# Kernel tuning notes

Hardware: AMD Instinct MI355X
Metric: run time of the kernel (lower is better)

The kernel has to match this reference:

```python
import jax, jax.numpy as jnp
import numpy as np

D = 768
H = 12
MLP = 3072
EPS = 1e-5


def _layernorm(x, g, b):
    mu = jnp.mean(x, axis=-1, keepdims=True)
    var = jnp.var(x, axis=-1, keepdims=True)
    return (x - mu) * jax.lax.rsqrt(var + EPS) * g + b


def setup_inputs() -> dict:
    key = jax.random.key(0)
    ks = jax.random.split(key, 16)
    s = 0.02
    inp = {
        "x": jax.random.normal(ks[0], (8, 1024, D), dtype=jnp.float32),
        "ln1_g": jnp.ones((D,), jnp.float32),
        "ln1_b": jnp.zeros((D,), jnp.float32),
        "Wq": jax.random.normal(ks[1], (D, D), jnp.float32) * s,
        "bq": jnp.zeros((D,), jnp.float32),
        "Wk": jax.random.normal(ks[2], (D, D), jnp.float32) * s,
        "bk": jnp.zeros((D,), jnp.float32),
        "Wv": jax.random.normal(ks[3], (D, D), jnp.float32) * s,
        "bv": jnp.zeros((D,), jnp.float32),
        "Wo": jax.random.normal(ks[4], (D, D), jnp.float32) * s,
        "bo": jnp.zeros((D,), jnp.float32),
        "ln2_g": jnp.ones((D,), jnp.float32),
        "ln2_b": jnp.zeros((D,), jnp.float32),
        "W1": jax.random.normal(ks[5], (D, MLP), jnp.float32) * s,
        "b1": jnp.zeros((MLP,), jnp.float32),
        "W2": jax.random.normal(ks[6], (MLP, D), jnp.float32) * s,
        "b2": jnp.zeros((D,), jnp.float32),
    }
    return inp


def reference(x, ln1_g, ln1_b, Wq, bq, Wk, bk, Wv, bv, Wo, bo, ln2_g, ln2_b, W1, b1, W2, b2):
    b, n, d = x.shape
    dh = d // H
    scale = 1.0 / jnp.sqrt(jnp.float32(d))  # NOTE: sqrt(input_dim), per source

    h = _layernorm(x, ln1_g, ln1_b)
    q = (h @ Wq + bq).reshape(b, n, H, dh).transpose(0, 2, 1, 3)  # bhnf
    k = (h @ Wk + bk).reshape(b, n, H, dh).transpose(0, 2, 1, 3)
    v = (h @ Wv + bv).reshape(b, n, H, dh).transpose(0, 2, 1, 3)

    score = jax.nn.softmax(jnp.einsum('bhif,bhjf->bhij', q, k) * scale, axis=-1)
    attn = jnp.einsum('bhij,bhjf->bihf', score, v).reshape(b, n, d)
    out = attn @ Wo + bo + x  # residual (dropout p=0)

    h2 = _layernorm(out, ln2_g, ln2_b)
    mlp = jax.nn.gelu(jax.nn.gelu(h2 @ W1 + b1, approximate=False) @ W2 + b2, approximate=False)
    return mlp + out
```

## Files before the change

kernel.cpp:

```cpp
#include <hip/hip_runtime.h>
#include <hip/hip_bf16.h>
#include <math.h>

typedef __bf16 bf16x8 __attribute__((ext_vector_type(8)));
typedef float f32x4 __attribute__((ext_vector_type(4)));

#define DD 768
#define HH 12
#define MLPD 3072
#define QSCALE 0.036084391824351615f

__device__ __forceinline__ float gelu_fast(float x) {
    float y = 1.5957691216057308f * x + 0.07135481283154893f * x * x * x;
    return x * __builtin_amdgcn_rcpf(1.0f + __expf(-y));
}

__device__ __forceinline__ void gload16(const void* g, void* l) {
    __builtin_amdgcn_global_load_lds(
        (const __attribute__((address_space(1))) unsigned int*)g,
        (__attribute__((address_space(3))) unsigned int*)l, 16, 0, 0);
}

__global__ __launch_bounds__(256) void wtrans_all(
    const float* __restrict__ Wq, const float* __restrict__ Wk,
    const float* __restrict__ Wv, const float* __restrict__ Wo,
    const float* __restrict__ W1, const float* __restrict__ W2,
    __bf16* __restrict__ wqkv, __bf16* __restrict__ wo,
    __bf16* __restrict__ w1, __bf16* __restrict__ w2) {
    __shared__ float tile[64][65];
    int b = blockIdx.x;
    const float* W; __bf16* Wt; int K, N, tk, tn;
    if (b < 432) {
        int wsel = b / 144, r = b - wsel * 144;
        W = wsel == 0 ? Wq : (wsel == 1 ? Wk : Wv);
        Wt = wqkv + (size_t)wsel * 768 * 768;
        K = 768; N = 768; tk = r % 12; tn = r / 12;
    } else if (b < 576) {
        int r = b - 432; W = Wo; Wt = wo; K = 768; N = 768; tk = r % 12; tn = r / 12;
    } else if (b < 1152) {
        int r = b - 576; W = W1; Wt = w1; K = 768; N = 3072; tk = r % 12; tn = r / 12;
    } else {
        int r = b - 1152; W = W2; Wt = w2; K = 3072; N = 768; tk = r % 48; tn = r / 48;
    }
    int k0 = tk * 64, n0 = tn * 64;
    int t = threadIdx.x;
    int tr = t >> 6, tc = t & 63;
#pragma unroll
    for (int i = 0; i < 16; ++i) {
        int row = i * 4 + tr;
        tile[row][tc] = W[(size_t)(k0 + row) * N + n0 + tc];
    }
    __syncthreads();
#pragma unroll
    for (int i = 0; i < 16; ++i) {
        int row = i * 4 + tr;
        Wt[(size_t)(n0 + row) * K + k0 + tc] = (__bf16)tile[tc][row];
    }
}

__global__ __launch_bounds__(64) void ln_kernel(const float* __restrict__ X,
                                                const float* __restrict__ g,
                                                const float* __restrict__ b,
                                                __bf16* __restrict__ O) {
    int row = blockIdx.x;
    int lane = threadIdx.x;
    const float* xr = X + (size_t)row * DD;
    float4 v[3];
    float s = 0.f, ss = 0.f;
#pragma unroll
    for (int i = 0; i < 3; ++i) {
        v[i] = *reinterpret_cast<const float4*>(&xr[(i * 64 + lane) * 4]);
        s += v[i].x + v[i].y + v[i].z + v[i].w;
        ss += v[i].x * v[i].x + v[i].y * v[i].y + v[i].z * v[i].z + v[i].w * v[i].w;
    }
#pragma unroll
    for (int m = 1; m < 64; m <<= 1) {
        s += __shfl_xor(s, m);
        ss += __shfl_xor(ss, m);
    }
    float mu = s * (1.0f / DD);
    float rstd = rsqrtf(ss * (1.0f / DD) - mu * mu + 1e-5f);
#pragma unroll
    for (int i = 0; i < 3; ++i) {
        int c = (i * 64 + lane) * 4;
        float4 gv = *reinterpret_cast<const float4*>(&g[c]);
        float4 bv = *reinterpret_cast<const float4*>(&b[c]);
        union { __bf16 h[4]; uint2 u; } o;
        o.h[0] = (__bf16)((v[i].x - mu) * rstd * gv.x + bv.x);
        o.h[1] = (__bf16)((v[i].y - mu) * rstd * gv.y + bv.y);
        o.h[2] = (__bf16)((v[i].z - mu) * rstd * gv.z + bv.z);
        o.h[3] = (__bf16)((v[i].w - mu) * rstd * gv.w + bv.w);
        *reinterpret_cast<uint2*>(&O[(size_t)row * DD + c]) = o.u;
    }
}

template <int EPI>
__global__ __launch_bounds__(512, 2) void gemm8(
    const __bf16* __restrict__ A, const __bf16* __restrict__ Bt,
    const float* __restrict__ b0, const float* __restrict__ b1, const float* __restrict__ b2,
    void* __restrict__ o0, void* __restrict__ o1, void* __restrict__ o2,
    int M, int N, int K) {
    extern __shared__ __bf16 lds[];
    __bf16* As = lds;
    __bf16* Bs = lds + 49152;
    const int t = threadIdx.x;
    const int w = t >> 6, lane = t & 63;
    const int wm = w >> 1, wn = w & 1;
    const int lr = lane & 15, lg = lane >> 4;
    const int m0 = blockIdx.x * 256, n0 = blockIdx.y * 128;
    const int lrow8 = lane >> 3;
    const int cSwz = ((lane & 7) ^ lrow8) * 8;

    const __bf16* aSrc = A + (size_t)(m0 + w * 32 + lrow8) * K + cSwz;
    const __bf16* bSrc = Bt + (size_t)(n0 + w * 16 + lrow8) * K + cSwz;
    const int ldsA = w * 32 * 64;
    const int ldsB = w * 16 * 64;

    const int nt = K >> 6;
    f32x4 acc[4][4] = {};

    auto stageA = [&](int T, int c) {
        gload16(aSrc + (size_t)(c * 8) * K + T * 64,
                &As[(T % 3) * 16384 + ldsA + c * 8 * 64]);
    };
    auto stageB = [&](int T, int c) {
        gload16(bSrc + (size_t)(c * 8) * K + T * 64,
                &Bs[(T % 3) * 8192 + ldsB + c * 8 * 64]);
    };

    for (int T = 0; T < 2; ++T) {
        stageA(T, 0); stageA(T, 1); stageA(T, 2); stageA(T, 3);
        stageB(T, 0); stageB(T, 1);
    }
    asm volatile("s_waitcnt vmcnt(6)" ::: "memory");
    __builtin_amdgcn_s_barrier();

    for (int T = 0; T < nt; ++T) {
        const int bufA = (T % 3) * 16384, bufB = (T % 3) * 8192;
#pragma unroll
        for (int kg = 0; kg < 2; ++kg) {
            bf16x8 af[4], bfr[4];
#pragma unroll
            for (int i = 0; i < 4; ++i)
                af[i] = *reinterpret_cast<const bf16x8*>(
                    &As[bufA + (wm * 64 + i * 16 + lr) * 64 + (((kg << 2) | lg) ^ (lr & 7)) * 8]);
#pragma unroll
            for (int j = 0; j < 4; ++j)
                bfr[j] = *reinterpret_cast<const bf16x8*>(
                    &Bs[bufB + (wn * 64 + j * 16 + lr) * 64 + (((kg << 2) | lg) ^ (lr & 7)) * 8]);
            if (T + 2 < nt) {
                stageA(T + 2, kg * 2); stageA(T + 2, kg * 2 + 1); stageB(T + 2, kg);
            }
            __builtin_amdgcn_s_barrier();
            asm volatile("s_waitcnt lgkmcnt(0)" ::: "memory");
            __builtin_amdgcn_sched_barrier(0);
            __builtin_amdgcn_s_setprio(1);
#pragma unroll
            for (int i = 0; i < 4; ++i)
#pragma unroll
                for (int j = 0; j < 4; ++j)
                    acc[i][j] = __builtin_amdgcn_mfma_f32_16x16x32_bf16(bfr[j], af[i], acc[i][j], 0, 0, 0);
            __builtin_amdgcn_s_setprio(0);
            if (kg == 1) {
                if (T < nt - 2) { asm volatile("s_waitcnt vmcnt(6)" ::: "memory"); }
                else            { asm volatile("s_waitcnt vmcnt(0)" ::: "memory"); }
            }
            __builtin_amdgcn_s_barrier();
        }
    }

#pragma unroll
    for (int i = 0; i < 4; ++i) {
        const int m = m0 + wm * 64 + i * 16 + lr;
        const int bI = m >> 10, ntok = m & 1023;
#pragma unroll
        for (int j = 0; j < 4; ++j) {
            const int n = n0 + wn * 64 + j * 16 + lg * 4;
            if (EPI == 0) {
                const int wid = n / 768;
                const int cc0 = n - wid * 768;
                const int hh = cc0 >> 6, f0 = cc0 & 63;
                const float* bsel = (wid == 0 ? b0 : (wid == 1 ? b1 : b2));
                const float4 bv = *reinterpret_cast<const float4*>(&bsel[cc0]);
                const float v0 = acc[i][j][0] + bv.x, v1 = acc[i][j][1] + bv.y;
                const float v2 = acc[i][j][2] + bv.z, v3 = acc[i][j][3] + bv.w;
                if (wid == 0) {
                    union { __bf16 h[4]; uint2 u; } pk;
                    pk.h[0] = (__bf16)(v0 * QSCALE); pk.h[1] = (__bf16)(v1 * QSCALE);
                    pk.h[2] = (__bf16)(v2 * QSCALE); pk.h[3] = (__bf16)(v3 * QSCALE);
                    *reinterpret_cast<uint2*>(
                        &((__bf16*)o0)[((((size_t)(bI * HH + hh) << 10) + ntok) << 6) + f0]) = pk.u;
                } else if (wid == 1) {
                    union { __bf16 h[4]; uint2 u; } pk;
                    pk.h[0] = (__bf16)v0; pk.h[1] = (__bf16)v1;
                    pk.h[2] = (__bf16)v2; pk.h[3] = (__bf16)v3;
                    *reinterpret_cast<uint2*>(
                        &((__bf16*)o1)[((((size_t)(bI * HH + hh) << 10) + ntok) << 6) + f0]) = pk.u;
                } else {
                    __bf16* vb = (__bf16*)o2;
                    size_t base = ((size_t)(bI * HH + hh) * 64 + f0) << 10;
                    vb[base + ntok] = (__bf16)v0;
                    vb[base + (1 << 10) + ntok] = (__bf16)v1;
                    vb[base + (2 << 10) + ntok] = (__bf16)v2;
                    vb[base + (3 << 10) + ntok] = (__bf16)v3;
                }
            } else {
                const float4 bv = *reinterpret_cast<const float4*>(&b0[n]);
                union { __bf16 h[4]; uint2 u; } pk;
                pk.h[0] = (__bf16)gelu_fast(acc[i][j][0] + bv.x);
                pk.h[1] = (__bf16)gelu_fast(acc[i][j][1] + bv.y);
                pk.h[2] = (__bf16)gelu_fast(acc[i][j][2] + bv.z);
                pk.h[3] = (__bf16)gelu_fast(acc[i][j][3] + bv.w);
                *reinterpret_cast<uint2*>(&((__bf16*)o0)[(size_t)m * MLPD + n]) = pk.u;
            }
        }
    }
}

template <int EPI, int BM>
__global__ __launch_bounds__(256) void gemm_bt(
    const __bf16* __restrict__ A, const __bf16* __restrict__ Bt,
    const float* __restrict__ b0, void* __restrict__ o0,
    const float* __restrict__ resid, int M, int N, int K) {
    constexpr int WCOLS = (BM == 128) ? 2 : 4;
    constexpr int SPAN = 128 / WCOLS;
    constexpr int NJ = SPAN / 16;
    __shared__ __bf16 As[BM * 64];
    __shared__ __bf16 Bs[128 * 64];
    const int t = threadIdx.x;
    const int m0 = blockIdx.x * BM, n0 = blockIdx.y * 128;
    const int w = t >> 6, lane = t & 63;
    const int wm = w / WCOLS, wn = w % WCOLS;
    const int lr = lane & 15, lg = lane >> 4;

    const int srow = w * 8 + (lane >> 3);
    const int scol = (lane & 7) * 8;
    const __bf16* aP = A + (size_t)(m0 + srow) * K + scol;
    const __bf16* bP = Bt + (size_t)(n0 + srow) * K + scol;
    const int lbase = w * 8 * 64;

    f32x4 acc[4][NJ] = {};

    for (int k0 = 0; k0 < K; k0 += 64) {
        __syncthreads();
#pragma unroll
        for (int c = 0; c < BM / 32; ++c)
            gload16(aP + (size_t)c * 32 * K + k0, &As[lbase + c * 2048]);
#pragma unroll
        for (int c = 0; c < 4; ++c)
            gload16(bP + (size_t)c * 32 * K + k0, &Bs[lbase + c * 2048]);
        __syncthreads();
#pragma unroll
        for (int kg = 0; kg < 2; ++kg) {
            bf16x8 af[4], bfr[NJ];
#pragma unroll
            for (int i = 0; i < 4; ++i)
                af[i] = *reinterpret_cast<const bf16x8*>(&As[(wm * 64 + i * 16 + lr) * 64 + kg * 32 + lg * 8]);
#pragma unroll
            for (int j = 0; j < NJ; ++j)
                bfr[j] = *reinterpret_cast<const bf16x8*>(&Bs[(wn * SPAN + j * 16 + lr) * 64 + kg * 32 + lg * 8]);
#pragma unroll
            for (int i = 0; i < 4; ++i)
#pragma unroll
                for (int j = 0; j < NJ; ++j)
                    acc[i][j] = __builtin_amdgcn_mfma_f32_16x16x32_bf16(bfr[j], af[i], acc[i][j], 0, 0, 0);
        }
    }

#pragma unroll
    for (int i = 0; i < 4; ++i) {
        const int m = m0 + wm * 64 + i * 16 + lr;
#pragma unroll
        for (int j = 0; j < NJ; ++j) {
            const int n = n0 + wn * SPAN + j * 16 + lg * 4;
            const float4 bv = *reinterpret_cast<const float4*>(&b0[n]);
            const float v0 = acc[i][j][0] + bv.x, v1 = acc[i][j][1] + bv.y;
            const float v2 = acc[i][j][2] + bv.z, v3 = acc[i][j][3] + bv.w;
            const float4 rv = *reinterpret_cast<const float4*>(&resid[(size_t)m * DD + n]);
            if (EPI == 2) {
                float4 ov = {v0 + rv.x, v1 + rv.y, v2 + rv.z, v3 + rv.w};
                *reinterpret_cast<float4*>(&((float*)o0)[(size_t)m * DD + n]) = ov;
            } else {
                float4 ov = {gelu_fast(v0) + rv.x, gelu_fast(v1) + rv.y,
                             gelu_fast(v2) + rv.z, gelu_fast(v3) + rv.w};
                *reinterpret_cast<float4*>(&((float*)o0)[(size_t)m * DD + n]) = ov;
            }
        }
    }
}

__global__ __launch_bounds__(512, 6) void attn_kernel(
    const __bf16* __restrict__ Q, const __bf16* __restrict__ Kg,
    const __bf16* __restrict__ Vt, __bf16* __restrict__ Aout) {
    __shared__ char KsB[2][64 * 128];
    __shared__ char VsB[2][64 * 128];
    __shared__ char PsB[8][16 * 128];
    const int id = blockIdx.x;
    const int swz = (id & 7) * 96 + (id >> 3);
    const int bh = swz >> 3, qt = swz & 7;
    const int t = threadIdx.x, w = t >> 6, lane = t & 63;
    const int lr = lane & 15, lg = lane >> 4;
    const size_t bhN = (size_t)bh << 10;
    const int q0 = qt * 128;

    bf16x8 qf[2];
#pragma unroll
    for (int kg = 0; kg < 2; ++kg)
        qf[kg] = *reinterpret_cast<const bf16x8*>(&Q[(bhN + q0 + w * 16 + lr) * 64 + kg * 32 + lg * 8]);

    const int srow = t >> 3;
    const int sc = ((t & 7) ^ (srow & 7)) * 16;
    const char* kbase = (const char*)Kg + bhN * 128;
    const char* vbase = (const char*)Vt + ((size_t)bh << 17);
    const int wlds = w * 1024;

    f32x4 oacc[4] = {};
    float lsum[4] = {0.f, 0.f, 0.f, 0.f};

    gload16(kbase + (size_t)srow * 128 + sc, KsB[0] + wlds);
    gload16(vbase + (size_t)srow * 2048 + sc, VsB[0] + wlds);

    for (int kt = 0; kt < 16; ++kt) {
        const int buf = kt & 1;
        if (kt < 15) {
            gload16(kbase + (size_t)((kt + 1) * 64 + srow) * 128 + sc, KsB[buf ^ 1] + wlds);
            gload16(vbase + (size_t)srow * 2048 + (kt + 1) * 128 + sc, VsB[buf ^ 1] + wlds);
            asm volatile("s_waitcnt vmcnt(2)" ::: "memory");
        } else {
            asm volatile("s_waitcnt vmcnt(0)" ::: "memory");
        }
        __builtin_amdgcn_s_barrier();

        f32x4 s[4] = {};
        __builtin_amdgcn_s_setprio(1);
#pragma unroll
        for (int kg = 0; kg < 2; ++kg) {
#pragma unroll
            for (int j = 0; j < 4; ++j) {
                int row = j * 16 + lr;
                bf16x8 kf = *reinterpret_cast<const bf16x8*>(
                    KsB[buf] + ((row * 128 + kg * 64 + lg * 16) ^ ((row & 7) << 4)));
                s[j] = __builtin_amdgcn_mfma_f32_16x16x32_bf16(qf[kg], kf, s[j], 0, 0, 0);
            }
        }
        __builtin_amdgcn_s_setprio(0);
#pragma unroll
        for (int r = 0; r < 4; ++r) {
            int prow = lg * 4 + r;
#pragma unroll
            for (int j = 0; j < 4; ++j) {
                float pv = __expf(s[j][r]);
                lsum[r] += pv;
                *reinterpret_cast<__bf16*>(
                    PsB[w] + ((prow * 128 + (j * 16 + lr) * 2) ^ ((prow & 7) << 4))) = (__bf16)pv;
            }
        }
        __builtin_amdgcn_s_setprio(1);
#pragma unroll
        for (int kg = 0; kg < 2; ++kg) {
            bf16x8 pf = *reinterpret_cast<const bf16x8*>(
                PsB[w] + ((lr * 128 + kg * 64 + lg * 16) ^ ((lr & 7) << 4)));
#pragma unroll
            for (int j = 0; j < 4; ++j) {
                int row = j * 16 + lr;
                bf16x8 vf = *reinterpret_cast<const bf16x8*>(
                    VsB[buf] + ((row * 128 + kg * 64 + lg * 16) ^ ((row & 7) << 4)));
                oacc[j] = __builtin_amdgcn_mfma_f32_16x16x32_bf16(pf, vf, oacc[j], 0, 0, 0);
            }
        }
        __builtin_amdgcn_s_setprio(0);
        __builtin_amdgcn_s_barrier();
    }

#pragma unroll
    for (int r = 0; r < 4; ++r)
#pragma unroll
        for (int m = 1; m < 16; m <<= 1) lsum[r] += __shfl_xor(lsum[r], m);

    const int bI = bh / HH, hh = bh % HH;
#pragma unroll
    for (int r = 0; r < 4; ++r) {
        float inv = 1.0f / lsum[r];
        int qrow = q0 + w * 16 + lg * 4 + r;
        size_t base = ((size_t)(bI << 10) + qrow) * DD + hh * 64;
#pragma unroll
        for (int j = 0; j < 4; ++j)
            Aout[base + j * 16 + lr] = (__bf16)(oacc[j][r] * inv);
    }
}

extern "C" void kernel_launch(void* const* d_in, const int* in_sizes, int n_in,
                              void* d_out, int out_size, void* d_ws, size_t ws_size,
                              hipStream_t stream) {
    const float* x     = (const float*)d_in[0];
    const float* ln1_g = (const float*)d_in[1];
    const float* ln1_b = (const float*)d_in[2];
    const float* Wq    = (const float*)d_in[3];
    const float* bq    = (const float*)d_in[4];
    const float* Wk    = (const float*)d_in[5];
    const float* bk    = (const float*)d_in[6];
    const float* Wv    = (const float*)d_in[7];
    const float* bv    = (const float*)d_in[8];
    const float* Wo    = (const float*)d_in[9];
    const float* bo    = (const float*)d_in[10];
    const float* ln2_g = (const float*)d_in[11];
    const float* ln2_b = (const float*)d_in[12];
    const float* W1    = (const float*)d_in[13];
    const float* b1    = (const float*)d_in[14];
    const float* W2    = (const float*)d_in[15];
    const float* b2    = (const float*)d_in[16];

    char* p = (char*)d_ws;
    auto alloc = [&](size_t bytes) { char* r = p; p += bytes; return r; };
    __bf16* wqkv_t = (__bf16*)alloc((size_t)2304 * 768 * 2);
    __bf16* wo_t   = (__bf16*)alloc((size_t)768 * 768 * 2);
    __bf16* w1_t   = (__bf16*)alloc((size_t)3072 * 768 * 2);
    __bf16* w2_t   = (__bf16*)alloc((size_t)768 * 3072 * 2);
    __bf16* h      = (__bf16*)alloc((size_t)8192 * 768 * 2);
    float*  outb   = (float*) alloc((size_t)8192 * 768 * 4);
    __bf16* q      = (__bf16*)alloc((size_t)8192 * 768 * 2);
    __bf16* kb     = (__bf16*)alloc((size_t)8192 * 768 * 2);
    __bf16* vt     = (__bf16*)alloc((size_t)8192 * 768 * 2);
    __bf16* attn   = (__bf16*)alloc((size_t)8192 * 768 * 2);
    __bf16* mid    = q;

    const int LDS8 = 147456;
    hipFuncSetAttribute(reinterpret_cast<const void*>(gemm8<0>),
                        hipFuncAttributeMaxDynamicSharedMemorySize, LDS8);
    hipFuncSetAttribute(reinterpret_cast<const void*>(gemm8<3>),
                        hipFuncAttributeMaxDynamicSharedMemorySize, LDS8);

    wtrans_all<<<1728, 256, 0, stream>>>(Wq, Wk, Wv, Wo, W1, W2, wqkv_t, wo_t, w1_t, w2_t);

    ln_kernel<<<8192, 64, 0, stream>>>(x, ln1_g, ln1_b, h);
    gemm8<0><<<dim3(32, 18), 512, LDS8, stream>>>(h, wqkv_t, bq, bk, bv, q, kb, vt,
                                                  8192, 2304, 768);
    attn_kernel<<<768, 512, 0, stream>>>(q, kb, vt, attn);
    gemm_bt<2, 64><<<dim3(128, 6), 256, 0, stream>>>(attn, wo_t, bo, outb, x, 8192, 768, 768);
    ln_kernel<<<8192, 64, 0, stream>>>(outb, ln2_g, ln2_b, h);
    gemm8<3><<<dim3(32, 24), 512, LDS8, stream>>>(h, w1_t, b1, nullptr, nullptr, mid,
                                                  nullptr, nullptr, 8192, 3072, 768);
    gemm_bt<4, 64><<<dim3(128, 6), 256, 0, stream>>>(mid, w2_t, b2, (float*)d_out, outb,
                                                     8192, 768, 3072);
}
```

Before: 263.9 us.

## Triple-buffer Wo/W2 GEMMs with async LDS loads, XOR swizzle, and 128x64 tiles

Replaces the single-buffered gemm_bt used for the output projection and second MLP GEMM with gemm_p2. The new kernel uses a 3-stage ring of global_load_lds buffers with loads issued two tiles ahead, vmcnt-based waits and barriers in place of full syncthreads, and an XOR swizzle on LDS columns to avoid bank conflicts. The tile shape changes from 64x128 to 128x64, with raised MFMA priority and two blocks per CU. The aim is to hide global memory latency behind MFMA work, at the cost of more LDS per block and more delicate synchronisation.

```diff
diff --git a/kernel.cpp b/kernel.cpp
--- a/kernel.cpp
+++ b/kernel.cpp
@@ -217,53 +217,77 @@
     }
 }
 
-template <int EPI, int BM>
-__global__ __launch_bounds__(256) void gemm_bt(
+template <int EPI>
+__global__ __launch_bounds__(256, 2) void gemm_p2(
     const __bf16* __restrict__ A, const __bf16* __restrict__ Bt,
     const float* __restrict__ b0, void* __restrict__ o0,
     const float* __restrict__ resid, int M, int N, int K) {
-    constexpr int WCOLS = (BM == 128) ? 2 : 4;
-    constexpr int SPAN = 128 / WCOLS;
-    constexpr int NJ = SPAN / 16;
-    __shared__ __bf16 As[BM * 64];
-    __shared__ __bf16 Bs[128 * 64];
+    extern __shared__ __bf16 lds[];
+    __bf16* As = lds;
+    __bf16* Bs = lds + 24576;
     const int t = threadIdx.x;
-    const int m0 = blockIdx.x * BM, n0 = blockIdx.y * 128;
     const int w = t >> 6, lane = t & 63;
-    const int wm = w / WCOLS, wn = w % WCOLS;
+    const int wm = w >> 1, wn = w & 1;
     const int lr = lane & 15, lg = lane >> 4;
-
-    const int srow = w * 8 + (lane >> 3);
-    const int scol = (lane & 7) * 8;
-    const __bf16* aP = A + (size_t)(m0 + srow) * K + scol;
-    const __bf16* bP = Bt + (size_t)(n0 + srow) * K + scol;
-    const int lbase = w * 8 * 64;
-
-    f32x4 acc[4][NJ] = {};
-
-    for (int k0 = 0; k0 < K; k0 += 64) {
-        __syncthreads();
-#pragma unroll
-        for (int c = 0; c < BM / 32; ++c)
-            gload16(aP + (size_t)c * 32 * K + k0, &As[lbase + c * 2048]);
-#pragma unroll
-        for (int c = 0; c < 4; ++c)
-            gload16(bP + (size_t)c * 32 * K + k0, &Bs[lbase + c * 2048]);
-        __syncthreads();
+    const int m0 = blockIdx.x * 128, n0 = blockIdx.y * 64;
+    const int lrow8 = lane >> 3;
+    const int cSwz = ((lane & 7) ^ lrow8) * 8;
+
+    const __bf16* aSrc = A + (size_t)(m0 + w * 32 + lrow8) * K + cSwz;
+    const __bf16* bSrc = Bt + (size_t)(n0 + w * 16 + lrow8) * K + cSwz;
+    const int ldsA = w * 32 * 64;
+    const int ldsB = w * 16 * 64;
+
+    const int nt = K >> 6;
+    f32x4 acc[4][2] = {};
+
+    auto stageA = [&](int T, int c) {
+        gload16(aSrc + (size_t)(c * 8) * K + T * 64,
+                &As[(T % 3) * 8192 + ldsA + c * 8 * 64]);
+    };
+    auto stageB = [&](int T, int c) {
+        gload16(bSrc + (size_t)(c * 8) * K + T * 64,
+                &Bs[(T % 3) * 4096 + ldsB + c * 8 * 64]);
+    };
+
+    for (int T = 0; T < 2; ++T) {
+        stageA(T, 0); stageA(T, 1); stageA(T, 2); stageA(T, 3);
+        stageB(T, 0); stageB(T, 1);
+    }
+    asm volatile("s_waitcnt vmcnt(6)" ::: "memory");
+    __builtin_amdgcn_s_barrier();
+
+    for (int T = 0; T < nt; ++T) {
+        const int bufA = (T % 3) * 8192, bufB = (T % 3) * 4096;
 #pragma unroll
         for (int kg = 0; kg < 2; ++kg) {
-            bf16x8 af[4], bfr[NJ];
+            bf16x8 af[4], bfr[2];
 #pragma unroll
             for (int i = 0; i < 4; ++i)
-                af[i] = *reinterpret_cast<const bf16x8*>(&As[(wm * 64 + i * 16 + lr) * 64 + kg * 32 + lg * 8]);
-#pragma unroll
-            for (int j = 0; j < NJ; ++j)
-                bfr[j] = *reinterpret_cast<const bf16x8*>(&Bs[(wn * SPAN + j * 16 + lr) * 64 + kg * 32 + lg * 8]);
+                af[i] = *reinterpret_cast<const bf16x8*>(
+                    &As[bufA + (wm * 64 + i * 16 + lr) * 64 + (((kg << 2) | lg) ^ (lr & 7)) * 8]);
+#pragma unroll
+            for (int j = 0; j < 2; ++j)
+                bfr[j] = *reinterpret_cast<const bf16x8*>(
+                    &Bs[bufB + (wn * 32 + j * 16 + lr) * 64 + (((kg << 2) | lg) ^ (lr & 7)) * 8]);
+            if (T + 2 < nt) {
+                stageA(T + 2, kg * 2); stageA(T + 2, kg * 2 + 1); stageB(T + 2, kg);
+            }
+            __builtin_amdgcn_s_barrier();
+            asm volatile("s_waitcnt lgkmcnt(0)" ::: "memory");
+            __builtin_amdgcn_sched_barrier(0);
+            __builtin_amdgcn_s_setprio(1);
 #pragma unroll
             for (int i = 0; i < 4; ++i)
 #pragma unroll
-                for (int j = 0; j < NJ; ++j)
+                for (int j = 0; j < 2; ++j)
                     acc[i][j] = __builtin_amdgcn_mfma_f32_16x16x32_bf16(bfr[j], af[i], acc[i][j], 0, 0, 0);
+            __builtin_amdgcn_s_setprio(0);
+            if (kg == 1) {
+                if (T < nt - 2) { asm volatile("s_waitcnt vmcnt(6)" ::: "memory"); }
+                else            { asm volatile("s_waitcnt vmcnt(0)" ::: "memory"); }
+            }
+            __builtin_amdgcn_s_barrier();
         }
     }
 
@@ -271,8 +295,8 @@
     for (int i = 0; i < 4; ++i) {
         const int m = m0 + wm * 64 + i * 16 + lr;
 #pragma unroll
-        for (int j = 0; j < NJ; ++j) {
-            const int n = n0 + wn * SPAN + j * 16 + lg * 4;
+        for (int j = 0; j < 2; ++j) {
+            const int n = n0 + wn * 32 + j * 16 + lg * 4;
             const float4 bv = *reinterpret_cast<const float4*>(&b0[n]);
             const float v0 = acc[i][j][0] + bv.x, v1 = acc[i][j][1] + bv.y;
             const float v2 = acc[i][j][2] + bv.z, v3 = acc[i][j][3] + bv.w;
@@ -425,10 +449,15 @@
     __bf16* mid    = q;
 
     const int LDS8 = 147456;
+    const int LDSP = 73728;
     hipFuncSetAttribute(reinterpret_cast<const void*>(gemm8<0>),
                         hipFuncAttributeMaxDynamicSharedMemorySize, LDS8);
     hipFuncSetAttribute(reinterpret_cast<const void*>(gemm8<3>),
                         hipFuncAttributeMaxDynamicSharedMemorySize, LDS8);
+    hipFuncSetAttribute(reinterpret_cast<const void*>(gemm_p2<2>),
+                        hipFuncAttributeMaxDynamicSharedMemorySize, LDSP);
+    hipFuncSetAttribute(reinterpret_cast<const void*>(gemm_p2<4>),
+                        hipFuncAttributeMaxDynamicSharedMemorySize, LDSP);
 
     wtrans_all<<<1728, 256, 0, stream>>>(Wq, Wk, Wv, Wo, W1, W2, wqkv_t, wo_t, w1_t, w2_t);
 
@@ -436,10 +465,10 @@
     gemm8<0><<<dim3(32, 18), 512, LDS8, stream>>>(h, wqkv_t, bq, bk, bv, q, kb, vt,
                                                   8192, 2304, 768);
     attn_kernel<<<768, 512, 0, stream>>>(q, kb, vt, attn);
-    gemm_bt<2, 64><<<dim3(128, 6), 256, 0, stream>>>(attn, wo_t, bo, outb, x, 8192, 768, 768);
+    gemm_p2<2><<<dim3(64, 12), 256, LDSP, stream>>>(attn, wo_t, bo, outb, x, 8192, 768, 768);
     ln_kernel<<<8192, 64, 0, stream>>>(outb, ln2_g, ln2_b, h);
     gemm8<3><<<dim3(32, 24), 512, LDS8, stream>>>(h, w1_t, b1, nullptr, nullptr, mid,
                                                   nullptr, nullptr, 8192, 3072, 768);
-    gemm_bt<4, 64><<<dim3(128, 6), 256, 0, stream>>>(mid, w2_t, b2, (float*)d_out, outb,
-                                                     8192, 768, 3072);
-}
+    gemm_p2<4><<<dim3(64, 12), 256, LDSP, stream>>>(mid, w2_t, b2, (float*)d_out, outb,
+                                                    8192, 768, 3072);
+}
```

Measured after the change: 257.6 us. -2.4%, faster.
